# Kernel tuning notes

Measured on AMD Instinct MI355X. Metric: run time of the kernel, lower is better.

The kernel has to match this reference:

```python
import jax, jax.numpy as jnp
import numpy as np

L = 2048         # new tokens (prefill)
HID = 4096
NH = 32          # attention heads
NKV = 8          # kv heads
HD = HID // NH   # 128
MAX = 4096       # kv-cache capacity
EPS = 1e-5


def _rope_tables(L, HD):
    inv_freq = 1.0 / (10000.0 ** (np.arange(0, HD, 2, dtype=np.float32) / HD))
    ang = np.arange(L, dtype=np.float32)[:, None] * inv_freq[None, :]  # [L, HD/2]
    ang = np.concatenate([ang, ang], axis=-1)                          # HF duplicated layout
    return jnp.asarray(np.cos(ang)), jnp.asarray(np.sin(ang))


def setup_inputs() -> dict:
    key = jax.random.key(0)
    ks = jax.random.split(key, 6)
    cos, sin = _rope_tables(L, HD)
    s = 0.02
    return {
        "x": jax.random.normal(ks[0], (L, HID), jnp.float32),
        "cos": cos,
        "sin": sin,
        "position_ids": jnp.arange(L, dtype=jnp.int64),
        "seq_len": L,
        "k_cache": jnp.zeros((MAX, NKV, HD), jnp.float32),
        "v_cache": jnp.zeros((MAX, NKV, HD), jnp.float32),
        "ln_w": jnp.ones((HID,), jnp.float32),
        "Wq": jax.random.normal(ks[1], (NH * HD, HID), jnp.float32) * s,
        "Wk": jax.random.normal(ks[2], (NKV * HD, HID), jnp.float32) * s,
        "Wv": jax.random.normal(ks[3], (NKV * HD, HID), jnp.float32) * s,
        "Wo": jax.random.normal(ks[4], (HID, NH * HD), jnp.float32) * s,
    }


def _rms_norm(x, w, eps=EPS):
    xf = x.astype(jnp.float32)
    var = jnp.mean(xf * xf, axis=-1, keepdims=True)
    return (w * (xf * jax.lax.rsqrt(var + eps))).astype(x.dtype)


def _rotate_half(x):
    x1, x2 = jnp.split(x, 2, axis=-1)
    return jnp.concatenate([-x2, x1], axis=-1)


def reference(x, cos, sin, position_ids, seq_len, k_cache, v_cache, ln_w, Wq, Wk, Wv, Wo):
    Lq, hid = x.shape
    nkv, hd = k_cache.shape[1], k_cache.shape[2]
    nh = Wq.shape[0] // hd
    g = nh // nkv

    residual = x
    h = _rms_norm(x, ln_w)

    q = (h @ Wq.T).reshape(Lq, nh, hd)
    k = (h @ Wk.T).reshape(Lq, nkv, hd)
    v = (h @ Wv.T).reshape(Lq, nkv, hd)

    # RoPE, cos/sin broadcast over heads (unsqueeze_dim=1)
    c = cos[:, None, :]
    s = sin[:, None, :]
    q = q * c + _rotate_half(q) * s
    k = k * c + _rotate_half(k) * s

    # KV-cache scatter write
    k_cache = k_cache.at[position_ids].set(k)
    v_cache = v_cache.at[position_ids].set(v)

    # prefill path (num_new_tokens > 1): causal GQA SDPA over new keys only
    scale = 1.0 / jnp.sqrt(jnp.asarray(hd, jnp.float32))
    qg = q.reshape(Lq, nkv, g, hd)
    scores = jnp.einsum('qhgd,khd->hgqk', qg, k) * scale  # [nkv, g, Lq, Lq]
    idx = jnp.arange(Lq)
    causal = idx[None, :] <= idx[:, None]                  # [Lq, Lq]
    scores = jnp.where(causal[None, None], scores, -jnp.inf)
    p = jax.nn.softmax(scores, axis=-1)
    attn = jnp.einsum('hgqk,khd->qhgd', p, v).reshape(Lq, nh * hd)

    out = residual + attn @ Wo.T
    return out, k_cache, v_cache
```

## Files before the change

### kernel.cpp

```cpp
#include <hip/hip_runtime.h>
#include <hip/hip_bf16.h>
#include <cstdint>

#define L_SEQ 2048
#define HID   4096
#define NH    32
#define NKV   8
#define HD    128
#define MAXP  4096
#define QKVD  6144
#define K_OFF 4096
#define V_OFF 5120

using bf16_t = __hip_bfloat16;
typedef __bf16 bf16x8 __attribute__((ext_vector_type(8)));
typedef float  f32x4  __attribute__((ext_vector_type(4)));
typedef short  short4v __attribute__((ext_vector_type(4)));
typedef short  short8v __attribute__((ext_vector_type(8)));

__device__ __forceinline__ void async_copy16(void* lds, const void* g) {
  __builtin_amdgcn_global_load_lds(
      (__attribute__((address_space(1))) void*)g,
      (__attribute__((address_space(3))) void*)lds, 16, 0, 0);
}

__device__ __forceinline__ f32x4 MFMA16(bf16x8 a, bf16x8 b, f32x4 c) {
  return __builtin_amdgcn_mfma_f32_16x16x32_bf16(a, b, c, 0, 0, 0);
}

__global__ __launch_bounds__(256) void rmsnorm_kernel(
    const float* __restrict__ x, const float* __restrict__ w,
    bf16_t* __restrict__ h) {
  int row = blockIdx.x, t = threadIdx.x;
  const float4* xv = (const float4*)(x + (size_t)row * HID);
  float4 v[4];
  float ss = 0.f;
#pragma unroll
  for (int i = 0; i < 4; i++) {
    v[i] = xv[i * 256 + t];
    ss += v[i].x * v[i].x + v[i].y * v[i].y + v[i].z * v[i].z + v[i].w * v[i].w;
  }
#pragma unroll
  for (int off = 32; off >= 1; off >>= 1) ss += __shfl_xor(ss, off, 64);
  __shared__ float red[4];
  if ((t & 63) == 0) red[t >> 6] = ss;
  __syncthreads();
  float rr = rsqrtf((red[0] + red[1] + red[2] + red[3]) * (1.0f / HID) + 1e-5f);
  const float4* wv = (const float4*)w;
  bf16_t* hr = h + (size_t)row * HID;
#pragma unroll
  for (int i = 0; i < 4; i++) {
    float4 wl = wv[i * 256 + t];
    bf16_t tmp[4];
    tmp[0] = __float2bfloat16(v[i].x * rr * wl.x);
    tmp[1] = __float2bfloat16(v[i].y * rr * wl.y);
    tmp[2] = __float2bfloat16(v[i].z * rr * wl.z);
    tmp[3] = __float2bfloat16(v[i].w * rr * wl.w);
    *(short4v*)(hr + (size_t)(i * 256 + t) * 4) = *(short4v*)tmp;
  }
}

__global__ __launch_bounds__(256) void cvt_bf16_kernel(
    const float* __restrict__ src, bf16_t* __restrict__ dst) {
  size_t i = ((size_t)blockIdx.x * 256 + threadIdx.x) * 8;
  float4 a = *(const float4*)(src + i);
  float4 b = *(const float4*)(src + i + 4);
  bf16_t tmp[8] = {__float2bfloat16(a.x), __float2bfloat16(a.y),
                   __float2bfloat16(a.z), __float2bfloat16(a.w),
                   __float2bfloat16(b.x), __float2bfloat16(b.y),
                   __float2bfloat16(b.z), __float2bfloat16(b.w)};
  *(short8v*)(dst + i) = *(short8v*)tmp;
}

template <int OUT_MODE>
__global__ __launch_bounds__(512) void gemm256_kernel(
    const bf16_t* __restrict__ A, const bf16_t* __restrict__ B,
    bf16_t* __restrict__ Cb, float* __restrict__ Cf,
    const float* __restrict__ resid, int N, int K) {
  __shared__ alignas(16) bf16_t As[2][2][128 * 64];
  __shared__ alignas(16) bf16_t Bs[2][2][128 * 64];

  const int t = threadIdx.x;
  const int l = t & 63;
  const int w = t >> 6;
  const int wm = w >> 2;
  const int wn = w & 3;
  const int wh = wn >> 1;
  const int wn1 = wn & 1;
  const int lane15 = l & 15, quad = l >> 4;
  const int l7 = l & 7;

  const bf16_t* Ag = A + (size_t)blockIdx.y * 256 * K;
  const bf16_t* Bg = B + (size_t)blockIdx.x * 256 * K;

  const int srow = t >> 3;
  const int sgran = (t & 7) ^ (srow & 7);
  const int wbase = w << 9;

#define STAGE(G, rowbase, kc, ldsh) do {                                      \
    const bf16_t* _g = (G) + (size_t)((rowbase) + srow) * K + (kc) + sgran * 8;\
    async_copy16((ldsh) + wbase, _g);                                         \
    async_copy16((ldsh) + wbase + 4096, _g + (size_t)64 * K);                 \
  } while (0)

#define VMW4() asm volatile("s_waitcnt vmcnt(4)" ::: "memory")
#define BAR() __builtin_amdgcn_s_barrier()

#define OFF(row, kk) (((row) * 64) + ((((kk) * 4 + quad) ^ l7) << 3))

#define RD_A(sl, ib) do { _Pragma("unroll")                                   \
    for (int i = 0; i < 4; i++) {                                             \
      a[i][0] = *(const bf16x8*)&As[sl][wm][OFF(((ib)+i) * 16 + lane15, 0)];  \
      a[i][1] = *(const bf16x8*)&As[sl][wm][OFF(((ib)+i) * 16 + lane15, 1)];  \
    } } while (0)

#define RD_B(sl, jb, dst) do { _Pragma("unroll")                              \
    for (int j = 0; j < 2; j++) {                                             \
      dst[j][0] = *(const bf16x8*)&Bs[sl][wh][OFF(wn1 * 64 + ((jb)+j) * 16 + lane15, 0)]; \
      dst[j][1] = *(const bf16x8*)&Bs[sl][wh][OFF(wn1 * 64 + ((jb)+j) * 16 + lane15, 1)]; \
    } } while (0)

#define MM(ib, jb, bsrc) do {                                                 \
    __builtin_amdgcn_s_setprio(1);                                            \
    _Pragma("unroll") for (int i = 0; i < 4; i++)                             \
    _Pragma("unroll") for (int j = 0; j < 2; j++) {                           \
      acc[(ib)+i][(jb)+j] = MFMA16(a[i][0], bsrc[j][0], acc[(ib)+i][(jb)+j]); \
      acc[(ib)+i][(jb)+j] = MFMA16(a[i][1], bsrc[j][1], acc[(ib)+i][(jb)+j]); \
    }                                                                         \
    __builtin_amdgcn_s_setprio(0);                                            \
  } while (0)

  STAGE(Bg, 0,   0,  &Bs[0][0][0]);
  STAGE(Ag, 0,   0,  &As[0][0][0]);
  STAGE(Bg, 128, 0,  &Bs[0][1][0]);
  STAGE(Ag, 128, 0,  &As[0][1][0]);
  STAGE(Bg, 0,   64, &Bs[1][0][0]);
  STAGE(Ag, 0,   64, &As[1][0][0]);
  VMW4();
  BAR();

  f32x4 acc[8][4] = {};
  bf16x8 a[4][2], blo[2][2], bhi[2][2];
  const int NTT = K >> 6;
  for (int it = 0; it < (NTT >> 1); ++it) {
    const int tb = it * 2;
    const int kc1 = (tb + 1) << 6;
    const int kc2 = ((tb + 2 < NTT) ? tb + 2 : NTT - 1) << 6;
    const int kc3 = ((tb + 3 < NTT) ? tb + 3 : NTT - 1) << 6;
    RD_A(0, 0); RD_B(0, 0, blo);
    STAGE(Bg, 128, kc1, &Bs[1][1][0]);
    BAR(); MM(0, 0, blo); BAR();
    RD_B(0, 2, bhi);
    STAGE(Ag, 128, kc1, &As[1][1][0]);
    BAR(); MM(0, 2, bhi); BAR();
    RD_A(0, 4);
    STAGE(Bg, 0, kc2, &Bs[0][0][0]);
    BAR(); MM(4, 0, blo); BAR();
    STAGE(Ag, 0, kc2, &As[0][0][0]);
    VMW4();
    BAR(); MM(4, 2, bhi); BAR();
    RD_A(1, 0); RD_B(1, 0, blo);
    STAGE(Bg, 128, kc2, &Bs[0][1][0]);
    BAR(); MM(0, 0, blo); BAR();
    RD_B(1, 2, bhi);
    STAGE(Ag, 128, kc2, &As[0][1][0]);
    BAR(); MM(0, 2, bhi); BAR();
    RD_A(1, 4);
    STAGE(Bg, 0, kc3, &Bs[1][0][0]);
    BAR(); MM(4, 0, blo); BAR();
    STAGE(Ag, 0, kc3, &As[1][0][0]);
    VMW4();
    BAR(); MM(4, 2, bhi); BAR();
  }

  const int row0 = blockIdx.y * 256 + wm * 128 + quad * 4;
  const int col0 = blockIdx.x * 256 + wn * 64 + lane15;
#pragma unroll
  for (int i = 0; i < 8; i++)
#pragma unroll
    for (int j = 0; j < 4; j++)
#pragma unroll
      for (int r = 0; r < 4; r++) {
        size_t idx = (size_t)(row0 + i * 16 + r) * N + col0 + j * 16;
        if (OUT_MODE == 0)
          Cb[idx] = __float2bfloat16(acc[i][j][r]);
        else
          Cf[idx] = acc[i][j][r] + resid[idx];
      }
#undef STAGE
#undef VMW4
#undef BAR
#undef OFF
#undef RD_A
#undef RD_B
#undef MM
}

__global__ __launch_bounds__(256) void rope_kernel(
    bf16_t* __restrict__ qkv,
    const float* __restrict__ cosT, const float* __restrict__ sinT,
    float* __restrict__ kc_out) {
  int idx = blockIdx.x * 256 + threadIdx.x;
  int d = idx & 63;
  int rest = idx >> 6;
  int hh = rest % (NH + NKV);
  int pos = rest / (NH + NKV);
  float c = cosT[pos * HD + d];
  float s = sinT[pos * HD + d];
  bf16_t* b = (hh < NH)
      ? qkv + (size_t)pos * QKVD + hh * HD
      : qkv + (size_t)pos * QKVD + K_OFF + (hh - NH) * HD;
  float x1 = __bfloat162float(b[d]);
  float x2 = __bfloat162float(b[d + 64]);
  float o1 = x1 * c - x2 * s;
  float o2 = x2 * c + x1 * s;
  b[d] = __float2bfloat16(o1);
  b[d + 64] = __float2bfloat16(o2);
  if (hh >= NH) {
    float* kc = kc_out + (size_t)pos * (NKV * HD) + (hh - NH) * HD;
    kc[d] = o1;
    kc[d + 64] = o2;
  }
}

__global__ __launch_bounds__(256) void vtrans_kernel(
    const bf16_t* __restrict__ qkv, float* __restrict__ vc_out,
    bf16_t* __restrict__ vT) {
  __shared__ alignas(16) short Ts[64 * 64];
  int kvh = blockIdx.x, pb = blockIdx.y, db = blockIdx.z;
  int t = threadIdx.x;
  int r = t & 63;
  int c4 = t >> 6;
  const short* src = (const short*)(qkv + (size_t)(pb * 64 + r) * QKVD +
                                    V_OFF + kvh * HD + db * 64 + c4 * 16);
  short8v v0 = *(const short8v*)src;
  short8v v1 = *(const short8v*)(src + 8);
  float* vo = vc_out + (size_t)(pb * 64 + r) * (NKV * HD) + kvh * HD + db * 64 + c4 * 16;
  float tmpf[16];
#pragma unroll
  for (int j = 0; j < 8; j++) {
    tmpf[j]     = __uint_as_float(((unsigned)(unsigned short)v0[j]) << 16);
    tmpf[j + 8] = __uint_as_float(((unsigned)(unsigned short)v1[j]) << 16);
  }
#pragma unroll
  for (int j = 0; j < 4; j++)
    ((float4*)vo)[j] = make_float4(tmpf[j * 4], tmpf[j * 4 + 1],
                                   tmpf[j * 4 + 2], tmpf[j * 4 + 3]);
  int cs = c4 ^ (r & 3);
  *(short8v*)&Ts[r * 64 + cs * 16] = v0;
  *(short8v*)&Ts[r * 64 + cs * 16 + 8] = v1;
  __syncthreads();
  int dr = t & 63;
  int pc = t >> 6;
  short vals[16];
#pragma unroll
  for (int j = 0; j < 16; j++) {
    int pos = pc * 16 + j;
    int cc = (dr >> 4) ^ (pos & 3);
    vals[j] = Ts[pos * 64 + cc * 16 + (dr & 15)];
  }
  short* dst = (short*)(vT + ((size_t)kvh * HD + db * 64 + dr) * L_SEQ + pb * 64 + pc * 16);
  *(short8v*)dst = *(short8v*)&vals[0];
  *(short8v*)(dst + 8) = *(short8v*)&vals[8];
}

__global__ __launch_bounds__(256) void cache_tail_kernel(
    const float* __restrict__ kc_in, const float* __restrict__ vc_in,
    float* __restrict__ kc_out, float* __restrict__ vc_out) {
  size_t base = (size_t)L_SEQ * NKV * HD;
  size_t i = base + ((size_t)blockIdx.x * 256 + threadIdx.x) * 4;
  *(float4*)(kc_out + i) = *(const float4*)(kc_in + i);
  *(float4*)(vc_out + i) = *(const float4*)(vc_in + i);
}

__global__ __launch_bounds__(256) void attn_kernel(
    const bf16_t* __restrict__ qkv, const bf16_t* __restrict__ vT,
    bf16_t* __restrict__ attn) {
  int h = blockIdx.x;
  int qblk = blockIdx.y;
  int kvh = h >> 2;
  int t = threadIdx.x, w = t >> 6, l = t & 63;
  int lane15 = l & 15, quad = l >> 4;

  __shared__ alignas(16) bf16_t Ks[16 * 512];
  __shared__ alignas(16) bf16_t Vs[16 * 512];
  __shared__ alignas(16) bf16_t Ps[4][32 * 68];

  bf16x8 aq[2][4];
#pragma unroll
  for (int i = 0; i < 2; i++)
#pragma unroll
    for (int kk = 0; kk < 4; kk++)
      aq[i][kk] = *(const bf16x8*)(qkv +
          (size_t)(qblk * 128 + w * 32 + i * 16 + lane15) * QKVD +
          h * HD + kk * 32 + quad * 8);

  f32x4 o[2][8] = {};
  float lsum[2][4] = {};
  const float scale = 0.08838834764831845f;
  int rowmax_w = qblk * 128 + w * 32 + 31;
  int nk = 2 * qblk + 2;

  for (int kblk = 0; kblk < nk; kblk++) {
    __syncthreads();
#pragma unroll
    for (int kk = 0; kk < 4; kk++)
      async_copy16(&Ks[(w * 4 + kk) * 512],
                   qkv + (size_t)(kblk * 64 + w * 16 + lane15) * QKVD +
                       K_OFF + kvh * HD + kk * 32 + quad * 8);
#pragma unroll
    for (int j = 0; j < 4; j++) {
      int tt = w * 2 + (j >> 1), kt2 = j & 1;
      async_copy16(&Vs[(tt * 2 + kt2) * 512],
                   vT + ((size_t)kvh * HD + tt * 16 + lane15) * L_SEQ +
                       kblk * 64 + kt2 * 32 + quad * 8);
    }
    __syncthreads();

    if (kblk * 64 <= rowmax_w) {
      f32x4 sacc[2][4] = {};
#pragma unroll
      for (int n = 0; n < 4; n++)
#pragma unroll
        for (int kk = 0; kk < 4; kk++) {
          bf16x8 b = *(const bf16x8*)&Ks[(n * 4 + kk) * 512 + l * 8];
          sacc[0][n] = __builtin_amdgcn_mfma_f32_16x16x32_bf16(aq[0][kk], b, sacc[0][n], 0, 0, 0);
          sacc[1][n] = __builtin_amdgcn_mfma_f32_16x16x32_bf16(aq[1][kk], b, sacc[1][n], 0, 0, 0);
        }
      bool maskblk = (kblk >= 2 * qblk);
#pragma unroll
      for (int i = 0; i < 2; i++)
#pragma unroll
        for (int n = 0; n < 4; n++) {
          int col = kblk * 64 + n * 16 + lane15;
#pragma unroll
          for (int r = 0; r < 4; r++) {
            float p = __expf(sacc[i][n][r] * scale);
            if (maskblk && col > (qblk * 128 + w * 32 + i * 16 + quad * 4 + r)) p = 0.f;
            lsum[i][r] += p;
            Ps[w][(i * 16 + quad * 4 + r) * 68 + n * 16 + lane15] = __float2bfloat16(p);
          }
        }
#pragma unroll
      for (int i = 0; i < 2; i++)
#pragma unroll
        for (int kt2 = 0; kt2 < 2; kt2++) {
          bf16x8 ap = *(const bf16x8*)&Ps[w][(i * 16 + lane15) * 68 + kt2 * 32 + quad * 8];
#pragma unroll
          for (int tt = 0; tt < 8; tt++) {
            bf16x8 b = *(const bf16x8*)&Vs[(tt * 2 + kt2) * 512 + l * 8];
            o[i][tt] = __builtin_amdgcn_mfma_f32_16x16x32_bf16(ap, b, o[i][tt], 0, 0, 0);
          }
        }
    }
  }

  float inv[2][4];
#pragma unroll
  for (int i = 0; i < 2; i++)
#pragma unroll
    for (int r = 0; r < 4; r++) {
      float s = lsum[i][r];
#pragma unroll
      for (int off = 1; off < 16; off <<= 1) s += __shfl_xor(s, off, 64);
      inv[i][r] = 1.f / s;
    }
  int qrow0 = qblk * 128 + w * 32;
#pragma unroll
  for (int i = 0; i < 2; i++)
#pragma unroll
    for (int tt = 0; tt < 8; tt++) {
      int col = h * HD + tt * 16 + lane15;
#pragma unroll
      for (int r = 0; r < 4; r++)
        attn[(size_t)(qrow0 + i * 16 + quad * 4 + r) * HID + col] =
            __float2bfloat16(o[i][tt][r] * inv[i][r]);
    }
}

extern "C" void kernel_launch(void* const* d_in, const int* in_sizes, int n_in,
                              void* d_out, int out_size, void* d_ws, size_t ws_size,
                              hipStream_t stream) {
  const float* x    = (const float*)d_in[0];
  const float* cosT = (const float*)d_in[1];
  const float* sinT = (const float*)d_in[2];
  const float* kc_in = (const float*)d_in[5];
  const float* vc_in = (const float*)d_in[6];
  const float* ln_w  = (const float*)d_in[7];
  const float* Wq = (const float*)d_in[8];
  const float* Wk = (const float*)d_in[9];
  const float* Wv = (const float*)d_in[10];
  const float* Wo = (const float*)d_in[11];

  float* out    = (float*)d_out;
  float* kc_out = out + (size_t)L_SEQ * HID;
  float* vc_out = kc_out + (size_t)MAXP * NKV * HD;

  char* ws = (char*)d_ws;
  bf16_t* h_bf    = (bf16_t*)(ws + 0);
  bf16_t* attn_bf = (bf16_t*)(ws + 0);
  bf16_t* Wqkv_bf = (bf16_t*)(ws + 16777216);
  bf16_t* Wo_bf   = (bf16_t*)(ws + 16777216);
  bf16_t* qkv_bf  = (bf16_t*)(ws + 67108864);
  bf16_t* vT_bf   = (bf16_t*)(ws + 92274688);

  rmsnorm_kernel<<<L_SEQ, 256, 0, stream>>>(x, ln_w, h_bf);
  cvt_bf16_kernel<<<(HID * HID) / (8 * 256), 256, 0, stream>>>(Wq, Wqkv_bf);
  cvt_bf16_kernel<<<(NKV * HD * HID) / (8 * 256), 256, 0, stream>>>(
      Wk, Wqkv_bf + (size_t)K_OFF * HID);
  cvt_bf16_kernel<<<(NKV * HD * HID) / (8 * 256), 256, 0, stream>>>(
      Wv, Wqkv_bf + (size_t)V_OFF * HID);

  gemm256_kernel<0><<<dim3(QKVD / 256, L_SEQ / 256), 512, 0, stream>>>(
      h_bf, Wqkv_bf, qkv_bf, nullptr, nullptr, QKVD, HID);

  rope_kernel<<<(L_SEQ * (NH + NKV) * 64) / 256, 256, 0, stream>>>(
      qkv_bf, cosT, sinT, kc_out);
  vtrans_kernel<<<dim3(NKV, L_SEQ / 64, HD / 64), 256, 0, stream>>>(
      qkv_bf, vc_out, vT_bf);
  cache_tail_kernel<<<((MAXP - L_SEQ) * NKV * HD) / (4 * 256), 256, 0, stream>>>(
      kc_in, vc_in, kc_out, vc_out);

  cvt_bf16_kernel<<<(HID * HID) / (8 * 256), 256, 0, stream>>>(Wo, Wo_bf);

  attn_kernel<<<dim3(NH, L_SEQ / 128), 256, 0, stream>>>(qkv_bf, vT_bf, attn_bf);

  gemm256_kernel<1><<<dim3(HID / 256, L_SEQ / 256), 512, 0, stream>>>(
      attn_bf, Wo_bf, nullptr, out, x, HID, HID);
}
```

Baseline: 625.7 us.

## Software-pipeline LDS fragment reads in GEMM with inline ds_read and lgkmcnt waits

Reworks the 256x256 bf16 GEMM main loop so the LDS fragment reads for the next MFMA quarter are issued before the current quarter's MFMAs. Partial s_waitcnt lgkmcnt waits let LDS latency overlap with matrix math. The reads use inline-asm ds_read_b128 with precomputed base pointers and immediate offsets, which cuts per-read address arithmetic. Launch bounds now request 2 blocks per CU, and a second A-fragment register set is added. The cost is higher register pressure and fragile hand-counted wait values.

```diff
diff --git a/kernel.cpp b/kernel.cpp
--- a/kernel.cpp
+++ b/kernel.cpp
@@ -72,13 +72,16 @@
   *(short8v*)(dst + i) = *(short8v*)tmp;
 }
 
+#define STR2_(x) #x
+#define STR_(x) STR2_(x)
+
 template <int OUT_MODE>
-__global__ __launch_bounds__(512) void gemm256_kernel(
+__global__ __launch_bounds__(512, 2) void gemm256_kernel(
     const bf16_t* __restrict__ A, const bf16_t* __restrict__ B,
     bf16_t* __restrict__ Cb, float* __restrict__ Cf,
     const float* __restrict__ resid, int N, int K) {
-  __shared__ alignas(16) bf16_t As[2][2][128 * 64];
-  __shared__ alignas(16) bf16_t Bs[2][2][128 * 64];
+  __shared__ alignas(16) bf16_t As[2 * 2 * 8192];
+  __shared__ alignas(16) bf16_t Bs[2 * 2 * 8192];
 
   const int t = threadIdx.x;
   const int l = t & 63;
@@ -97,81 +100,139 @@
   const int sgran = (t & 7) ^ (srow & 7);
   const int wbase = w << 9;
 
-#define STAGE(G, rowbase, kc, ldsh) do {                                      \
-    const bf16_t* _g = (G) + (size_t)((rowbase) + srow) * K + (kc) + sgran * 8;\
+  const bf16_t* pAg = Ag + (size_t)srow * K + sgran * 8;
+  const bf16_t* pBg = Bg + (size_t)srow * K + sgran * 8;
+  const size_t row64 = (size_t)64 * K;
+
+#define STAGE(PL, UOFF, ldsh) do {                                            \
+    const bf16_t* _g = (PL) + (UOFF);                                         \
     async_copy16((ldsh) + wbase, _g);                                         \
-    async_copy16((ldsh) + wbase + 4096, _g + (size_t)64 * K);                 \
+    async_copy16((ldsh) + wbase + 4096, _g + row64);                          \
   } while (0)
 
-#define VMW4() asm volatile("s_waitcnt vmcnt(4)" ::: "memory")
-#define BAR() __builtin_amdgcn_s_barrier()
-
-#define OFF(row, kk) (((row) * 64) + ((((kk) * 4 + quad) ^ l7) << 3))
-
-#define RD_A(sl, ib) do { _Pragma("unroll")                                   \
-    for (int i = 0; i < 4; i++) {                                             \
-      a[i][0] = *(const bf16x8*)&As[sl][wm][OFF(((ib)+i) * 16 + lane15, 0)];  \
-      a[i][1] = *(const bf16x8*)&As[sl][wm][OFF(((ib)+i) * 16 + lane15, 1)];  \
-    } } while (0)
-
-#define RD_B(sl, jb, dst) do { _Pragma("unroll")                              \
-    for (int j = 0; j < 2; j++) {                                             \
-      dst[j][0] = *(const bf16x8*)&Bs[sl][wh][OFF(wn1 * 64 + ((jb)+j) * 16 + lane15, 0)]; \
-      dst[j][1] = *(const bf16x8*)&Bs[sl][wh][OFF(wn1 * 64 + ((jb)+j) * 16 + lane15, 1)]; \
-    } } while (0)
-
-#define MM(ib, jb, bsrc) do {                                                 \
+#define ASD(sl, h) (&As[(sl) * 16384 + (h) * 8192])
+#define BSD(sl, h) (&Bs[(sl) * 16384 + (h) * 8192])
+
+  typedef __attribute__((address_space(3))) char* lds_b;
+  lds_b asb = (lds_b)As;
+  lds_b bsb = (lds_b)Bs;
+  const unsigned aoff0 = (unsigned)(wm * 16384 + lane15 * 128 + ((quad ^ l7) << 4));
+  const unsigned boff0 = (unsigned)(wh * 16384 + (wn1 * 64 + lane15) * 128 + ((quad ^ l7) << 4));
+  lds_b pa0s0 = asb + aoff0;
+  lds_b pa1s0 = asb + (aoff0 ^ 64u);
+  lds_b pa0s1 = pa0s0 + 32768;
+  lds_b pa1s1 = pa1s0 + 32768;
+  lds_b pb0s0 = bsb + boff0;
+  lds_b pb1s0 = bsb + (boff0 ^ 64u);
+  lds_b pb0s1 = pb0s0 + 32768;
+  lds_b pb1s1 = pb1s0 + 32768;
+
+#define DSR(dst, p, IMM) \
+  asm volatile("ds_read_b128 %0, %1 offset:" STR_(IMM) : "=v"(dst) : "v"(p))
+
+#define RA(dst, P0, P1, I0, I1, I2, I3) do {                                  \
+    DSR(dst[0][0], P0, I0); DSR(dst[0][1], P1, I0);                           \
+    DSR(dst[1][0], P0, I1); DSR(dst[1][1], P1, I1);                           \
+    DSR(dst[2][0], P0, I2); DSR(dst[2][1], P1, I2);                           \
+    DSR(dst[3][0], P0, I3); DSR(dst[3][1], P1, I3); } while (0)
+#define RB(dst, P0, P1, I0, I1) do {                                          \
+    DSR(dst[0][0], P0, I0); DSR(dst[0][1], P1, I0);                           \
+    DSR(dst[1][0], P0, I1); DSR(dst[1][1], P1, I1); } while (0)
+
+#define BAR() do { asm volatile("s_barrier");                                 \
+    __builtin_amdgcn_sched_barrier(0); } while (0)
+#define LGKM(NW) do { asm volatile("s_waitcnt lgkmcnt(" STR_(NW) ")");        \
+    __builtin_amdgcn_sched_barrier(0); } while (0)
+#define VMW(NW) asm volatile("s_waitcnt vmcnt(" STR_(NW) ")")
+
+#define MMQ(IB, JB, AF, BF) do {                                              \
     __builtin_amdgcn_s_setprio(1);                                            \
     _Pragma("unroll") for (int i = 0; i < 4; i++)                             \
     _Pragma("unroll") for (int j = 0; j < 2; j++) {                           \
-      acc[(ib)+i][(jb)+j] = MFMA16(a[i][0], bsrc[j][0], acc[(ib)+i][(jb)+j]); \
-      acc[(ib)+i][(jb)+j] = MFMA16(a[i][1], bsrc[j][1], acc[(ib)+i][(jb)+j]); \
+      acc[(IB)+i][(JB)+j] = MFMA16(AF[i][0], BF[j][0], acc[(IB)+i][(JB)+j]);  \
+      acc[(IB)+i][(JB)+j] = MFMA16(AF[i][1], BF[j][1], acc[(IB)+i][(JB)+j]);  \
     }                                                                         \
     __builtin_amdgcn_s_setprio(0);                                            \
+    __builtin_amdgcn_sched_barrier(0);                                        \
   } while (0)
 
-  STAGE(Bg, 0,   0,  &Bs[0][0][0]);
-  STAGE(Ag, 0,   0,  &As[0][0][0]);
-  STAGE(Bg, 128, 0,  &Bs[0][1][0]);
-  STAGE(Ag, 128, 0,  &As[0][1][0]);
-  STAGE(Bg, 0,   64, &Bs[1][0][0]);
-  STAGE(Ag, 0,   64, &As[1][0][0]);
-  VMW4();
+  const size_t u128 = (size_t)128 * K;
+  const int NTT = K >> 6;
+  const int niter = NTT >> 1;
+
+  f32x4 acc[8][4] = {};
+  bf16x8 a[4][2], a2[4][2], blo[2][2], bhi[2][2];
+
+  STAGE(pBg, 0,          BSD(0, 0));
+  STAGE(pAg, 0,          ASD(0, 0));
+  STAGE(pBg, u128,       BSD(0, 1));
+  STAGE(pAg, u128,       ASD(0, 1));
+  STAGE(pBg, 64,         BSD(1, 0));
+  STAGE(pAg, 64,         ASD(1, 0));
+  VMW(4);
   BAR();
-
-  f32x4 acc[8][4] = {};
-  bf16x8 a[4][2], blo[2][2], bhi[2][2];
-  const int NTT = K >> 6;
-  for (int it = 0; it < (NTT >> 1); ++it) {
+  RA(a, pa0s0, pa1s0, 0, 2048, 4096, 6144);
+  RB(blo, pb0s0, pb1s0, 0, 2048);
+
+  for (int it = 0; it < niter; ++it) {
     const int tb = it * 2;
-    const int kc1 = (tb + 1) << 6;
-    const int kc2 = ((tb + 2 < NTT) ? tb + 2 : NTT - 1) << 6;
-    const int kc3 = ((tb + 3 < NTT) ? tb + 3 : NTT - 1) << 6;
-    RD_A(0, 0); RD_B(0, 0, blo);
-    STAGE(Bg, 128, kc1, &Bs[1][1][0]);
-    BAR(); MM(0, 0, blo); BAR();
-    RD_B(0, 2, bhi);
-    STAGE(Ag, 128, kc1, &As[1][1][0]);
-    BAR(); MM(0, 2, bhi); BAR();
-    RD_A(0, 4);
-    STAGE(Bg, 0, kc2, &Bs[0][0][0]);
-    BAR(); MM(4, 0, blo); BAR();
-    STAGE(Ag, 0, kc2, &As[0][0][0]);
-    VMW4();
-    BAR(); MM(4, 2, bhi); BAR();
-    RD_A(1, 0); RD_B(1, 0, blo);
-    STAGE(Bg, 128, kc2, &Bs[0][1][0]);
-    BAR(); MM(0, 0, blo); BAR();
-    RD_B(1, 2, bhi);
-    STAGE(Ag, 128, kc2, &As[0][1][0]);
-    BAR(); MM(0, 2, bhi); BAR();
-    RD_A(1, 4);
-    STAGE(Bg, 0, kc3, &Bs[1][0][0]);
-    BAR(); MM(4, 0, blo); BAR();
-    STAGE(Ag, 0, kc3, &As[1][0][0]);
-    VMW4();
-    BAR(); MM(4, 2, bhi); BAR();
-  }
+    const size_t kc1 = (size_t)((tb + 1) << 6);
+    const size_t kc2 = (size_t)(((tb + 2 < NTT) ? tb + 2 : NTT - 1) << 6);
+    const size_t kc3 = (size_t)(((tb + 3 < NTT) ? tb + 3 : NTT - 1) << 6);
+    STAGE(pBg, u128 + kc1, BSD(1, 1));
+    BAR();
+    RB(bhi, pb0s0, pb1s0, 4096, 6144);
+    LGKM(4);
+    MMQ(0, 0, a, blo);
+    BAR();
+    STAGE(pAg, u128 + kc1, ASD(1, 1));
+    BAR();
+    RA(a2, pa0s0, pa1s0, 8192, 10240, 12288, 14336);
+    LGKM(8);
+    MMQ(0, 2, a, bhi);
+    BAR();
+    STAGE(pBg, kc2, BSD(0, 0));
+    BAR();
+    LGKM(0);
+    MMQ(4, 0, a2, blo);
+    BAR();
+    STAGE(pAg, kc2, ASD(0, 0));
+    VMW(4);
+    BAR();
+    RA(a, pa0s1, pa1s1, 0, 2048, 4096, 6144);
+    RB(blo, pb0s1, pb1s1, 0, 2048);
+    LGKM(12);
+    MMQ(4, 2, a2, bhi);
+    BAR();
+    STAGE(pBg, u128 + kc2, BSD(0, 1));
+    BAR();
+    RB(bhi, pb0s1, pb1s1, 4096, 6144);
+    LGKM(4);
+    MMQ(0, 0, a, blo);
+    BAR();
+    STAGE(pAg, u128 + kc2, ASD(0, 1));
+    BAR();
+    RA(a2, pa0s1, pa1s1, 8192, 10240, 12288, 14336);
+    LGKM(8);
+    MMQ(0, 2, a, bhi);
+    BAR();
+    STAGE(pBg, kc3, BSD(1, 0));
+    BAR();
+    LGKM(0);
+    MMQ(4, 0, a2, blo);
+    BAR();
+    STAGE(pAg, kc3, ASD(1, 0));
+    VMW(4);
+    BAR();
+    if (it + 1 < niter) {
+      RA(a, pa0s0, pa1s0, 0, 2048, 4096, 6144);
+      RB(blo, pb0s0, pb1s0, 0, 2048);
+    }
+    LGKM(12);
+    MMQ(4, 2, a2, bhi);
+    BAR();
+  }
+  VMW(0);
 
   const int row0 = blockIdx.y * 256 + wm * 128 + quad * 4;
   const int col0 = blockIdx.x * 256 + wn * 64 + lane15;
@@ -188,12 +249,15 @@
           Cf[idx] = acc[i][j][r] + resid[idx];
       }
 #undef STAGE
-#undef VMW4
+#undef ASD
+#undef BSD
+#undef DSR
+#undef RA
+#undef RB
 #undef BAR
-#undef OFF
-#undef RD_A
-#undef RD_B
-#undef MM
+#undef LGKM
+#undef VMW
+#undef MMQ
 }
 
 __global__ __launch_bounds__(256) void rope_kernel(
```

Result: faster. 575.6 us (-8.0%).
